# Kernel tuning notes

Hardware: AMD Instinct MI355X
Metric: run time of the kernel (lower is better)

The kernel has to match this reference:

```python
import jax, jax.numpy as jnp
import numpy as np

C = 128        # attention channels (inner_channel)
OUT_C = 256    # bottleneck output channels (in_channel)
NEG = -10000000.0


def conv_bn_relu(x, W, scale, shift):
    """1x1 conv (no bias) + eval-mode BatchNorm folded to scale/shift + ReLU.
    x: [B, Cin, H, W], W: [Cout, Cin]."""
    y = jnp.einsum('oc,bchw->bohw', W, x)
    y = y * scale[None, :, None, None] + shift[None, :, None, None]
    return jax.nn.relu(y)


def setup_inputs() -> dict:
    key = jax.random.key(0)
    ks = jax.random.split(key, 20)
    B, H, W_, K = 4, 128, 128, 1024
    inp = {
        'query_feats': jax.random.normal(ks[0], (B, C, H, W_), jnp.float32),
        'key_feats':   jax.random.normal(ks[1], (B, C, K, 1), jnp.float32),
        'value_feats': jax.random.normal(ks[2], (B, C, K, 1), jnp.float32),
        'key_mask':    jax.random.randint(ks[3], (B, 1, K, 1), 0, 2).astype(bool),
    }
    s = 1.0 / np.sqrt(C)

    def mk(i, cin, cout):
        return (jax.random.normal(ks[i], (cout, cin), jnp.float32) * s,
                jnp.ones((cout,), jnp.float32),
                jnp.zeros((cout,), jnp.float32))

    inp['Wq1'], inp['sq1'], inp['bq1'] = mk(4, C, C)
    inp['Wq2'], inp['sq2'], inp['bq2'] = mk(5, C, C)
    inp['Wk1'], inp['sk1'], inp['bk1'] = mk(6, C, C)
    inp['Wk2'], inp['sk2'], inp['bk2'] = mk(7, C, C)
    inp['Wv'],  inp['sv'],  inp['bv']  = mk(8, C, C)
    inp['Wo'],  inp['so'],  inp['bo']  = mk(9, C, C)
    inp['Wb'],  inp['sb'],  inp['bb']  = mk(10, 2 * C, OUT_C)
    return inp


def reference(query_feats, key_feats, value_feats, key_mask,
              Wq1, sq1, bq1, Wq2, sq2, bq2,
              Wk1, sk1, bk1, Wk2, sk2, bk2,
              Wv, sv, bv, Wo, so, bo, Wb, sb, bb):
    B, _, H, W_ = query_feats.shape
    # projections (2 conv-bn-relu for q/k, 1 for v)
    q = conv_bn_relu(conv_bn_relu(query_feats, Wq1, sq1, bq1), Wq2, sq2, bq2)
    k = conv_bn_relu(conv_bn_relu(key_feats, Wk1, sk1, bk1), Wk2, sk2, bk2)
    v = conv_bn_relu(value_feats, Wv, sv, bv)

    q = q.reshape(B, C, -1).transpose(0, 2, 1)   # [B, HW, C]
    k = k.reshape(B, C, -1)                      # [B, C, K]
    v = v.reshape(B, C, -1).transpose(0, 2, 1)   # [B, K, C]

    sim = jnp.einsum('bqc,bck->bqk', q, k) * (C ** -0.5)   # [B, HW, K]
    m = key_mask.reshape(B, 1, -1).astype(sim.dtype)        # [B, 1, K]
    sim = sim * m + NEG * (1.0 - m)
    attn = jax.nn.softmax(sim, axis=-1)

    ctx = jnp.einsum('bqk,bkc->bqc', attn, v)               # [B, HW, C]
    ctx = ctx.transpose(0, 2, 1).reshape(B, C, H, W_)
    ctx = conv_bn_relu(ctx, Wo, so, bo)                     # out_project

    out = conv_bn_relu(jnp.concatenate([ctx, query_feats], axis=1), Wb, sb, bb)
    return out
```

## Files before the change

### kernel.cpp

```cpp
#include <hip/hip_runtime.h>
#include <hip/hip_bf16.h>

#define B_    4
#define C_    128
#define HW_   16384
#define K_    1024
#define SC2_  0.12751734f
#define NEGL_ (-1.4427e7f)
#define DTHR_ 8.0f

using bf16 = __hip_bfloat16;
typedef __bf16 b8v __attribute__((ext_vector_type(8)));
typedef __bf16 b4v __attribute__((ext_vector_type(4)));
typedef __bf16 b2v __attribute__((ext_vector_type(2)));
typedef float  f4v __attribute__((ext_vector_type(4)));

__device__ __forceinline__ b8v ldb8(const void* p) { return *(const b8v*)p; }
__device__ __forceinline__ b4v ldb4(const void* p) { return *(const b4v*)p; }

#define XSTRIDE 272
#define KSTRIDE 272
#define VSTRIDE 136

__device__ __forceinline__ b8v ldw8(const float* wp, float sc) {
    const float4 a = *(const float4*)wp;
    const float4 c = *(const float4*)(wp + 4);
    b8v r;
    r[0] = (__bf16)(a.x * sc); r[1] = (__bf16)(a.y * sc);
    r[2] = (__bf16)(a.z * sc); r[3] = (__bf16)(a.w * sc);
    r[4] = (__bf16)(c.x * sc); r[5] = (__bf16)(c.y * sc);
    r[6] = (__bf16)(c.z * sc); r[7] = (__bf16)(c.w * sc);
    return r;
}

__global__ __launch_bounds__(256, 2) void prep_kernel(
    const float* __restrict__ query, const float* __restrict__ key, const float* __restrict__ val,
    const float* __restrict__ Wq1, const float* __restrict__ sq1,
    const float* __restrict__ Wq2, const float* __restrict__ sq2,
    const float* __restrict__ Wo,  const float* __restrict__ so,
    const float* __restrict__ Wb,  const float* __restrict__ sb,
    const float* __restrict__ Wk1, const float* __restrict__ sk1, const float* __restrict__ bk1,
    const float* __restrict__ Wk2, const float* __restrict__ sk2, const float* __restrict__ bk2,
    const float* __restrict__ Wv,  const float* __restrict__ sv_, const float* __restrict__ bv,
    bf16* __restrict__ qt, bf16* __restrict__ kbuf, bf16* __restrict__ vbuf,
    __bf16* __restrict__ Wq1p, __bf16* __restrict__ Wq2p,
    __bf16* __restrict__ Wop,  __bf16* __restrict__ Wbp)
{
    __shared__ __align__(16) char SM[69632];
    const int blk = blockIdx.x, t = threadIdx.x;

    if (blk < 32) {
        const int b = blk >> 3, n0 = (blk & 7) * 128;
        const int w = t >> 6, lane = t & 63;
        const int pl = lane & 15, quad = lane >> 4;
        const int ob = 32 * w;
        const int plT = t & 63, cg = t >> 6;
        char*    Xs  = SM;
        __bf16*  Ys  = (__bf16*)(SM + 34816);
        float*   Tmp = (float*)(SM + 34816);

        auto transpose_in = [&](const float* src) {
#pragma unroll
            for (int h = 0; h < 2; ++h) {
                const int p0 = n0 + h * 64;
#pragma unroll 4
                for (int i2 = 0; i2 < 32; ++i2) {
                    const int c = cg * 32 + i2;
                    Tmp[plT * 129 + c] = src[(size_t)(b * 128 + c) * K_ + p0 + plT];
                }
                __syncthreads();
#pragma unroll 4
                for (int it = 0; it < 16; ++it) {
                    const int p = it * 4 + cg;
                    b2v pk2;
                    pk2[0] = (__bf16)Tmp[p * 129 + 2 * plT];
                    pk2[1] = (__bf16)Tmp[p * 129 + 2 * plT + 1];
                    *(b2v*)(Xs + (h * 64 + p) * XSTRIDE + 4 * plT) = pk2;
                }
                __syncthreads();
            }
        };

        transpose_in(key);
        b8v W1f[2][4], W2f[2][4];
#pragma unroll
        for (int mt = 0; mt < 2; ++mt)
#pragma unroll
            for (int s = 0; s < 4; ++s) {
                const int row = ob + mt * 16 + pl;
                W1f[mt][s] = ldw8(Wk1 + row * 128 + s * 32 + quad * 8, sk1[row]);
                W2f[mt][s] = ldw8(Wk2 + row * 128 + s * 32 + quad * 8, sk2[row]);
            }
        {
            f4v acc[2][8];
#pragma unroll
            for (int mt = 0; mt < 2; ++mt)
#pragma unroll
                for (int nt = 0; nt < 8; ++nt) acc[mt][nt] = (f4v){0.f, 0.f, 0.f, 0.f};
#pragma unroll
            for (int s = 0; s < 4; ++s) {
                b8v Bf[8];
#pragma unroll
                for (int nt = 0; nt < 8; ++nt)
                    Bf[nt] = ldb8(Xs + (nt * 16 + pl) * XSTRIDE + s * 64 + quad * 16);
#pragma unroll
                for (int mt = 0; mt < 2; ++mt)
#pragma unroll
                    for (int nt = 0; nt < 8; ++nt)
                        acc[mt][nt] = __builtin_amdgcn_mfma_f32_16x16x32_bf16(W1f[mt][s], Bf[nt], acc[mt][nt], 0, 0, 0);
            }
#pragma unroll
            for (int mt = 0; mt < 2; ++mt) {
                const float4 s4 = *(const float4*)(bk1 + ob + mt * 16 + quad * 4);
                const float shf[4] = {s4.x, s4.y, s4.z, s4.w};
#pragma unroll
                for (int nt = 0; nt < 8; ++nt) {
                    b4v y;
#pragma unroll
                    for (int r = 0; r < 4; ++r) y[r] = (__bf16)fmaxf(acc[mt][nt][r] + shf[r], 0.f);
                    *(b4v*)&Ys[(nt * 16 + pl) * 136 + ob + mt * 16 + quad * 4] = y;
                }
            }
        }
        __syncthreads();
        {
            f4v acc2[2][8];
#pragma unroll
            for (int mt = 0; mt < 2; ++mt)
#pragma unroll
                for (int nt = 0; nt < 8; ++nt) acc2[mt][nt] = (f4v){0.f, 0.f, 0.f, 0.f};
#pragma unroll
            for (int s = 0; s < 4; ++s) {
                b8v Bf[8];
#pragma unroll
                for (int nt = 0; nt < 8; ++nt)
                    Bf[nt] = *(const b8v*)&Ys[(nt * 16 + pl) * 136 + s * 32 + quad * 8];
#pragma unroll
                for (int mt = 0; mt < 2; ++mt)
#pragma unroll
                    for (int nt = 0; nt < 8; ++nt)
                        acc2[mt][nt] = __builtin_amdgcn_mfma_f32_16x16x32_bf16(W2f[mt][s], Bf[nt], acc2[mt][nt], 0, 0, 0);
            }
            bf16* kdst = kbuf + ((size_t)b * K_ + n0) * 128;
#pragma unroll
            for (int mt = 0; mt < 2; ++mt) {
                const float4 s4 = *(const float4*)(bk2 + ob + mt * 16 + quad * 4);
                const float shf[4] = {s4.x, s4.y, s4.z, s4.w};
#pragma unroll
                for (int nt = 0; nt < 8; ++nt) {
                    b4v y;
#pragma unroll
                    for (int r = 0; r < 4; ++r) y[r] = (__bf16)fmaxf(acc2[mt][nt][r] + shf[r], 0.f);
                    *(b4v*)(kdst + (size_t)(nt * 16 + pl) * 128 + ob + mt * 16 + quad * 4) = y;
                }
            }
        }
        __syncthreads();

        transpose_in(val);
        b8v Wvf[2][4];
#pragma unroll
        for (int mt = 0; mt < 2; ++mt)
#pragma unroll
            for (int s = 0; s < 4; ++s) {
                const int row = ob + mt * 16 + pl;
                Wvf[mt][s] = ldw8(Wv + row * 128 + s * 32 + quad * 8, sv_[row]);
            }
        {
            f4v acc[2][8];
#pragma unroll
            for (int mt = 0; mt < 2; ++mt)
#pragma unroll
                for (int nt = 0; nt < 8; ++nt) acc[mt][nt] = (f4v){0.f, 0.f, 0.f, 0.f};
#pragma unroll
            for (int s = 0; s < 4; ++s) {
                b8v Bf[8];
#pragma unroll
                for (int nt = 0; nt < 8; ++nt)
                    Bf[nt] = ldb8(Xs + (nt * 16 + pl) * XSTRIDE + s * 64 + quad * 16);
#pragma unroll
                for (int mt = 0; mt < 2; ++mt)
#pragma unroll
                    for (int nt = 0; nt < 8; ++nt)
                        acc[mt][nt] = __builtin_amdgcn_mfma_f32_16x16x32_bf16(Wvf[mt][s], Bf[nt], acc[mt][nt], 0, 0, 0);
            }
            bf16* vdst = vbuf + (size_t)b * 128 * K_;
#pragma unroll
            for (int mt = 0; mt < 2; ++mt) {
                const float4 s4 = *(const float4*)(bv + ob + mt * 16 + quad * 4);
                const float shf[4] = {s4.x, s4.y, s4.z, s4.w};
#pragma unroll
                for (int nt = 0; nt < 8; ++nt)
#pragma unroll
                    for (int r = 0; r < 4; ++r)
                        vdst[(size_t)(ob + mt * 16 + quad * 4 + r) * K_ + n0 + nt * 16 + pl]
                            = __float2bfloat16(fmaxf(acc[mt][nt][r] + shf[r], 0.f));
            }
        }
    } else if (blk < 1056) {
        float* Xs2 = (float*)SM;
        const int i = blk - 32;
        const int b = i >> 8, p0 = (i & 255) * 64;
        const int pl = t & 63, cg = t >> 6;
#pragma unroll 4
        for (int i2 = 0; i2 < 32; ++i2) {
            const int c = cg * 32 + i2;
            Xs2[pl * 129 + c] = query[(size_t)(b * 128 + c) * HW_ + p0 + pl];
        }
        __syncthreads();
#pragma unroll 4
        for (int it = 0; it < 16; ++it) {
            const int p = it * 4 + cg;
            b2v pk2;
            pk2[0] = (__bf16)Xs2[p * 129 + 2 * pl];
            pk2[1] = (__bf16)Xs2[p * 129 + 2 * pl + 1];
            *(b2v*)(qt + ((size_t)b * HW_ + p0 + p) * 128 + 2 * pl) = pk2;
        }
    } else {
        const int idx = (blk - 1056) * 256 + t;
        if (idx < 16384)      { Wq1p[idx] = (__bf16)(Wq1[idx] * sq1[idx >> 7]); }
        else if (idx < 32768) { const int i2 = idx - 16384; Wq2p[i2] = (__bf16)(Wq2[i2] * sq2[i2 >> 7]); }
        else if (idx < 49152) { const int i2 = idx - 32768; Wop[i2]  = (__bf16)(Wo[i2]  * so[i2 >> 7]); }
        else                  { const int i2 = idx - 49152; Wbp[i2]  = (__bf16)(Wb[i2]  * sb[i2 >> 8]); }
    }
}

__global__ __launch_bounds__(256, 2) void mega_kernel(
    const bf16* __restrict__ qt, const bf16* __restrict__ kbuf, const bf16* __restrict__ vbuf,
    const int* __restrict__ mask,
    const __bf16* __restrict__ Wq1p, const float* __restrict__ bq1,
    const __bf16* __restrict__ Wq2p, const float* __restrict__ bq2,
    const __bf16* __restrict__ Wop,  const float* __restrict__ bo,
    const __bf16* __restrict__ Wbp,  const float* __restrict__ bb,
    float* __restrict__ out)
{
    __shared__ __align__(16) char S[69632];

    const int t = threadIdx.x, w = t >> 6, lane = t & 63;
    const int pl = lane & 15, quad = lane >> 4;
    const int n0 = blockIdx.x * 128;
    const int b  = blockIdx.y;
    const int ob = 32 * w;

    char*   RA  = S;
    __bf16* RAh = (__bf16*)S;
    __bf16* RBh = (__bf16*)(S + 34816);
    char* xl = RA + (t >> 4) * XSTRIDE + (t & 15) * 16;

    {
        const char* qg = (const char*)(qt + ((size_t)b * HW_ + n0) * 128) + t * 16;
#pragma unroll
        for (int i = 0; i < 8; ++i)
            *(float4*)(xl + i * 16 * XSTRIDE) = *(const float4*)(qg + i * 4096);
    }
    {
        b8v W1f[2][4], W2f[2][4];
#pragma unroll
        for (int mt = 0; mt < 2; ++mt)
#pragma unroll
            for (int s = 0; s < 4; ++s) {
                W1f[mt][s] = ldb8(Wq1p + (ob + mt * 16 + pl) * 128 + s * 32 + quad * 8);
                W2f[mt][s] = ldb8(Wq2p + (ob + mt * 16 + pl) * 128 + s * 32 + quad * 8);
            }
        __syncthreads();

        f4v a1[2][8];
#pragma unroll
        for (int mt = 0; mt < 2; ++mt)
#pragma unroll
            for (int nt = 0; nt < 8; ++nt) a1[mt][nt] = (f4v){0.f, 0.f, 0.f, 0.f};
#pragma unroll
        for (int s = 0; s < 4; ++s) {
            b8v Bf[8];
#pragma unroll
            for (int nt = 0; nt < 8; ++nt)
                Bf[nt] = ldb8(RA + (nt * 16 + pl) * XSTRIDE + s * 64 + quad * 16);
#pragma unroll
            for (int mt = 0; mt < 2; ++mt)
#pragma unroll
                for (int nt = 0; nt < 8; ++nt)
                    a1[mt][nt] = __builtin_amdgcn_mfma_f32_16x16x32_bf16(W1f[mt][s], Bf[nt], a1[mt][nt], 0, 0, 0);
        }
#pragma unroll
        for (int mt = 0; mt < 2; ++mt) {
            const float4 s4 = *(const float4*)(bq1 + ob + mt * 16 + quad * 4);
            const float shf[4] = {s4.x, s4.y, s4.z, s4.w};
#pragma unroll
            for (int nt = 0; nt < 8; ++nt) {
                b4v y;
#pragma unroll
                for (int r = 0; r < 4; ++r) y[r] = (__bf16)fmaxf(a1[mt][nt][r] + shf[r], 0.f);
                *(b4v*)&RBh[(nt * 16 + pl) * 136 + ob + mt * 16 + quad * 4] = y;
            }
        }
        __syncthreads();

        f4v a2[2][8];
#pragma unroll
        for (int mt = 0; mt < 2; ++mt)
#pragma unroll
            for (int nt = 0; nt < 8; ++nt) a2[mt][nt] = (f4v){0.f, 0.f, 0.f, 0.f};
#pragma unroll
        for (int s = 0; s < 4; ++s) {
            b8v Bf[8];
#pragma unroll
            for (int nt = 0; nt < 8; ++nt)
                Bf[nt] = *(const b8v*)&RBh[(nt * 16 + pl) * 136 + s * 32 + quad * 8];
#pragma unroll
            for (int mt = 0; mt < 2; ++mt)
#pragma unroll
                for (int nt = 0; nt < 8; ++nt)
                    a2[mt][nt] = __builtin_amdgcn_mfma_f32_16x16x32_bf16(W2f[mt][s], Bf[nt], a2[mt][nt], 0, 0, 0);
        }
#pragma unroll
        for (int mt = 0; mt < 2; ++mt) {
            const float4 s4 = *(const float4*)(bq2 + ob + mt * 16 + quad * 4);
            const float shf[4] = {s4.x, s4.y, s4.z, s4.w};
#pragma unroll
            for (int nt = 0; nt < 8; ++nt) {
                b4v y;
#pragma unroll
                for (int r = 0; r < 4; ++r) y[r] = (__bf16)fmaxf(a2[mt][nt][r] + shf[r], 0.f);
                *(b4v*)&RAh[(nt * 16 + pl) * 136 + ob + mt * 16 + quad * 4] = y;
            }
        }
        __syncthreads();
    }

    b8v qf0[4], qf1[4];
#pragma unroll
    for (int s = 0; s < 4; ++s) {
        qf0[s] = ldb8(RA + (w * 32 + pl) * XSTRIDE + s * 64 + quad * 16);
        qf1[s] = ldb8(RA + (w * 32 + 16 + pl) * XSTRIDE + s * 64 + quad * 16);
    }
    __syncthreads();

    float* bias = (float*)S;
    char* ktile = S + 4096;
    char* vtile = S + 34816;

    for (int i2 = t; i2 < K_; i2 += 256)
        bias[i2] = (mask[b * K_ + i2] != 0) ? 0.f : NEGL_;

    const bf16* kpt = kbuf + (size_t)b * K_ * 128;
    const bf16* vpt = vbuf + (size_t)b * 128 * K_;
    const char* kg = (const char*)kpt + t * 16;
    const char* vg = (const char*)(vpt + (size_t)(t >> 3) * K_) + (t & 7) * 16;
    char* kl = ktile + (t >> 4) * KSTRIDE + (t & 15) * 16;
    char* vl = vtile + (t >> 3) * VSTRIDE + (t & 7) * 16;

    float4 k_r0 = *(const float4*)(kg);
    float4 k_r1 = *(const float4*)(kg + 4096);
    float4 k_r2 = *(const float4*)(kg + 8192);
    float4 k_r3 = *(const float4*)(kg + 12288);
    float4 v_r0 = *(const float4*)(vg);
    float4 v_r1 = *(const float4*)(vg + 65536);
    float4 v_r2 = *(const float4*)(vg + 131072);
    float4 v_r3 = *(const float4*)(vg + 196608);

    f4v ac0[8], ac1[8];
#pragma unroll
    for (int i = 0; i < 8; ++i) { ac0[i] = (f4v){0.f,0.f,0.f,0.f}; ac1[i] = (f4v){0.f,0.f,0.f,0.f}; }
    float mrun0 = -3.0e38f, mrun1 = -3.0e38f, lrun0 = 0.f, lrun1 = 0.f;

#define RAW_BARRIER()                                                 \
    __builtin_amdgcn_sched_barrier(0);                                \
    asm volatile("s_waitcnt lgkmcnt(0)" ::: "memory");                \
    __builtin_amdgcn_s_barrier();                                     \
    __builtin_amdgcn_sched_barrier(0);

    for (int chunk = 0; chunk < 16; ++chunk) {
        const int k0 = chunk * 64;

        *(float4*)(kl)                = k_r0;
        *(float4*)(kl + 16 * KSTRIDE) = k_r1;
        *(float4*)(kl + 32 * KSTRIDE) = k_r2;
        *(float4*)(kl + 48 * KSTRIDE) = k_r3;
        *(float4*)(vl)                = v_r0;
        *(float4*)(vl + 32 * VSTRIDE) = v_r1;
        *(float4*)(vl + 64 * VSTRIDE) = v_r2;
        *(float4*)(vl + 96 * VSTRIDE) = v_r3;
        RAW_BARRIER()

        if (chunk < 15) {
            const char* kgn = kg + (chunk + 1) * 16384;
            const char* vgn = vg + (chunk + 1) * 128;
            k_r0 = *(const float4*)(kgn);
            k_r1 = *(const float4*)(kgn + 4096);
            k_r2 = *(const float4*)(kgn + 8192);
            k_r3 = *(const float4*)(kgn + 12288);
            v_r0 = *(const float4*)(vgn);
            v_r1 = *(const float4*)(vgn + 65536);
            v_r2 = *(const float4*)(vgn + 131072);
            v_r3 = *(const float4*)(vgn + 196608);
        }

        f4v sv0[4], sv1[4];
        __builtin_amdgcn_s_setprio(1);
#pragma unroll
        for (int kt = 0; kt < 4; ++kt) {
            f4v a0 = (f4v){0.f,0.f,0.f,0.f}, a1 = (f4v){0.f,0.f,0.f,0.f};
            const char* krow = ktile + (kt * 16 + pl) * KSTRIDE + quad * 16;
#pragma unroll
            for (int s = 0; s < 4; ++s) {
                const b8v kf = ldb8(krow + s * 64);
                a0 = __builtin_amdgcn_mfma_f32_16x16x32_bf16(kf, qf0[s], a0, 0, 0, 0);
                a1 = __builtin_amdgcn_mfma_f32_16x16x32_bf16(kf, qf1[s], a1, 0, 0, 0);
            }
            const float4 b4 = *(const float4*)&bias[k0 + kt * 16 + quad * 4];
            const float bb4[4] = {b4.x, b4.y, b4.z, b4.w};
#pragma unroll
            for (int r = 0; r < 4; ++r) { sv0[kt][r] = a0[r] * SC2_ + bb4[r];
                                          sv1[kt][r] = a1[r] * SC2_ + bb4[r]; }
        }
        __builtin_amdgcn_s_setprio(0);

        float ml0 = sv0[0][0], ml1 = sv1[0][0];
#pragma unroll
        for (int kt = 0; kt < 4; ++kt)
#pragma unroll
            for (int r = 0; r < 4; ++r) { ml0 = fmaxf(ml0, sv0[kt][r]); ml1 = fmaxf(ml1, sv1[kt][r]); }
        ml0 = fmaxf(ml0, __shfl_xor(ml0, 16, 64)); ml0 = fmaxf(ml0, __shfl_xor(ml0, 32, 64));
        ml1 = fmaxf(ml1, __shfl_xor(ml1, 16, 64)); ml1 = fmaxf(ml1, __shfl_xor(ml1, 32, 64));

        if (__any((ml0 > mrun0 + DTHR_) || (ml1 > mrun1 + DTHR_))) {
            const float mn0 = fmaxf(mrun0, ml0), mn1 = fmaxf(mrun1, ml1);
            const float al0 = exp2f(mrun0 - mn0), al1 = exp2f(mrun1 - mn1);
            lrun0 *= al0; lrun1 *= al1;
            mrun0 = mn0;  mrun1 = mn1;
            float ar0[4], ar1[4];
#pragma unroll
            for (int r = 0; r < 4; ++r) { ar0[r] = __shfl(al0, quad * 4 + r, 64);
                                          ar1[r] = __shfl(al1, quad * 4 + r, 64); }
#pragma unroll
            for (int ct = 0; ct < 8; ++ct)
#pragma unroll
                for (int r = 0; r < 4; ++r) { ac0[ct][r] *= ar0[r]; ac1[ct][r] *= ar1[r]; }
        }

        b4v pk0[4], pk1[4];
        float rs0 = 0.f, rs1 = 0.f;
#pragma unroll
        for (int kt = 0; kt < 4; ++kt)
#pragma unroll
            for (int r = 0; r < 4; ++r) {
                const float p0 = exp2f(sv0[kt][r] - mrun0); rs0 += p0; pk0[kt][r] = (__bf16)p0;
                const float p1 = exp2f(sv1[kt][r] - mrun1); rs1 += p1; pk1[kt][r] = (__bf16)p1;
            }
        rs0 += __shfl_xor(rs0, 16, 64); rs0 += __shfl_xor(rs0, 32, 64);
        rs1 += __shfl_xor(rs1, 16, 64); rs1 += __shfl_xor(rs1, 32, 64);
        lrun0 += rs0; lrun1 += rs1;

        const b8v A00 = __builtin_shufflevector(pk0[0], pk0[1], 0, 1, 2, 3, 4, 5, 6, 7);
        const b8v A01 = __builtin_shufflevector(pk0[2], pk0[3], 0, 1, 2, 3, 4, 5, 6, 7);
        const b8v A10 = __builtin_shufflevector(pk1[0], pk1[1], 0, 1, 2, 3, 4, 5, 6, 7);
        const b8v A11 = __builtin_shufflevector(pk1[2], pk1[3], 0, 1, 2, 3, 4, 5, 6, 7);
        __builtin_amdgcn_s_setprio(1);
#pragma unroll
        for (int ct = 0; ct < 8; ++ct) {
            const char* vrow = vtile + (ct * 16 + pl) * VSTRIDE + quad * 8;
            const b8v B0 = __builtin_shufflevector(ldb4(vrow),      ldb4(vrow + 32), 0, 1, 2, 3, 4, 5, 6, 7);
            const b8v B1 = __builtin_shufflevector(ldb4(vrow + 64), ldb4(vrow + 96), 0, 1, 2, 3, 4, 5, 6, 7);
            ac0[ct] = __builtin_amdgcn_mfma_f32_16x16x32_bf16(A00, B0, ac0[ct], 0, 0, 0);
            ac0[ct] = __builtin_amdgcn_mfma_f32_16x16x32_bf16(A01, B1, ac0[ct], 0, 0, 0);
            ac1[ct] = __builtin_amdgcn_mfma_f32_16x16x32_bf16(A10, B0, ac1[ct], 0, 0, 0);
            ac1[ct] = __builtin_amdgcn_mfma_f32_16x16x32_bf16(A11, B1, ac1[ct], 0, 0, 0);
        }
        __builtin_amdgcn_s_setprio(0);

        RAW_BARRIER()
    }
#undef RAW_BARRIER

    {
        float inv0[4], inv1[4];
#pragma unroll
        for (int r = 0; r < 4; ++r) { inv0[r] = 1.f / __shfl(lrun0, quad * 4 + r, 64);
                                      inv1[r] = 1.f / __shfl(lrun1, quad * 4 + r, 64); }
#pragma unroll
        for (int ct = 0; ct < 8; ++ct)
#pragma unroll
            for (int r = 0; r < 4; ++r) {
                RAh[(w * 32 + quad * 4 + r) * 136 + ct * 16 + pl]      = (__bf16)(ac0[ct][r] * inv0[r]);
                RAh[(w * 32 + 16 + quad * 4 + r) * 136 + ct * 16 + pl] = (__bf16)(ac1[ct][r] * inv1[r]);
            }
    }
    __syncthreads();

    b8v Wof[2][4];
#pragma unroll
    for (int mt = 0; mt < 2; ++mt)
#pragma unroll
        for (int s = 0; s < 4; ++s)
            Wof[mt][s] = ldb8(Wop + (ob + mt * 16 + pl) * 128 + s * 32 + quad * 8);

    const char* qg2 = (const char*)(qt + ((size_t)b * HW_ + n0) * 128) + t * 16;
    float4 q_s0 = *(const float4*)(qg2);
    float4 q_s1 = *(const float4*)(qg2 + 4096);
    float4 q_s2 = *(const float4*)(qg2 + 8192);
    float4 q_s3 = *(const float4*)(qg2 + 12288);
    float4 q_s4 = *(const float4*)(qg2 + 16384);
    float4 q_s5 = *(const float4*)(qg2 + 20480);
    float4 q_s6 = *(const float4*)(qg2 + 24576);
    float4 q_s7 = *(const float4*)(qg2 + 28672);

    {
        f4v f1[2][8];
#pragma unroll
        for (int mt = 0; mt < 2; ++mt)
#pragma unroll
            for (int nt = 0; nt < 8; ++nt) f1[mt][nt] = (f4v){0.f, 0.f, 0.f, 0.f};
#pragma unroll
        for (int s = 0; s < 4; ++s) {
            b8v Bf[8];
#pragma unroll
            for (int nt = 0; nt < 8; ++nt)
                Bf[nt] = ldb8(RA + (nt * 16 + pl) * XSTRIDE + s * 64 + quad * 16);
#pragma unroll
            for (int mt = 0; mt < 2; ++mt)
#pragma unroll
                for (int nt = 0; nt < 8; ++nt)
                    f1[mt][nt] = __builtin_amdgcn_mfma_f32_16x16x32_bf16(Wof[mt][s], Bf[nt], f1[mt][nt], 0, 0, 0);
        }
#pragma unroll
        for (int mt = 0; mt < 2; ++mt) {
            const float4 s4 = *(const float4*)(bo + ob + mt * 16 + quad * 4);
            const float shf[4] = {s4.x, s4.y, s4.z, s4.w};
#pragma unroll
            for (int nt = 0; nt < 8; ++nt) {
                b4v y;
#pragma unroll
                for (int r = 0; r < 4; ++r) y[r] = (__bf16)fmaxf(f1[mt][nt][r] + shf[r], 0.f);
                *(b4v*)&RBh[(nt * 16 + pl) * 136 + ob + mt * 16 + quad * 4] = y;
            }
        }
    }
    __syncthreads();

    *(float4*)(xl)                 = q_s0;
    *(float4*)(xl + 16 * XSTRIDE)  = q_s1;
    *(float4*)(xl + 32 * XSTRIDE)  = q_s2;
    *(float4*)(xl + 48 * XSTRIDE)  = q_s3;
    *(float4*)(xl + 64 * XSTRIDE)  = q_s4;
    *(float4*)(xl + 80 * XSTRIDE)  = q_s5;
    *(float4*)(xl + 96 * XSTRIDE)  = q_s6;
    *(float4*)(xl + 112 * XSTRIDE) = q_s7;
    __syncthreads();

    {
        f4v f2[4][8];
#pragma unroll
        for (int mt = 0; mt < 4; ++mt)
#pragma unroll
            for (int nt = 0; nt < 8; ++nt) f2[mt][nt] = (f4v){0.f, 0.f, 0.f, 0.f};
#pragma unroll
        for (int ks = 0; ks < 8; ++ks) {
            b8v Af[4];
#pragma unroll
            for (int mt = 0; mt < 4; ++mt)
                Af[mt] = ldb8(Wbp + (size_t)(64 * w + mt * 16 + pl) * 256 + ks * 32 + quad * 8);
            b8v Bf[8];
            if (ks < 4) {
#pragma unroll
                for (int nt = 0; nt < 8; ++nt)
                    Bf[nt] = *(const b8v*)&RBh[(nt * 16 + pl) * 136 + ks * 32 + quad * 8];
            } else {
#pragma unroll
                for (int nt = 0; nt < 8; ++nt)
                    Bf[nt] = ldb8(RA + (nt * 16 + pl) * XSTRIDE + (ks - 4) * 64 + quad * 16);
            }
#pragma unroll
            for (int mt = 0; mt < 4; ++mt)
#pragma unroll
                for (int nt = 0; nt < 8; ++nt)
                    f2[mt][nt] = __builtin_amdgcn_mfma_f32_16x16x32_bf16(Af[mt], Bf[nt], f2[mt][nt], 0, 0, 0);
        }
#pragma unroll
        for (int mt = 0; mt < 4; ++mt) {
            const float4 s4 = *(const float4*)(bb + 64 * w + mt * 16 + quad * 4);
            const float shf[4] = {s4.x, s4.y, s4.z, s4.w};
#pragma unroll
            for (int nt = 0; nt < 8; ++nt)
#pragma unroll
                for (int r = 0; r < 4; ++r)
                    out[(size_t)(b * 256 + 64 * w + mt * 16 + quad * 4 + r) * HW_ + n0 + nt * 16 + pl]
                        = fmaxf(f2[mt][nt][r] + shf[r], 0.f);
        }
    }
}

extern "C" void kernel_launch(void* const* d_in, const int* in_sizes, int n_in,
                              void* d_out, int out_size, void* d_ws, size_t ws_size,
                              hipStream_t stream)
{
    const float* query = (const float*)d_in[0];
    const float* key   = (const float*)d_in[1];
    const float* val   = (const float*)d_in[2];
    const int*   mask  = (const int*)  d_in[3];
    const float* Wq1 = (const float*)d_in[4];  const float* sq1 = (const float*)d_in[5];  const float* bq1 = (const float*)d_in[6];
    const float* Wq2 = (const float*)d_in[7];  const float* sq2 = (const float*)d_in[8];  const float* bq2 = (const float*)d_in[9];
    const float* Wk1 = (const float*)d_in[10]; const float* sk1 = (const float*)d_in[11]; const float* bk1 = (const float*)d_in[12];
    const float* Wk2 = (const float*)d_in[13]; const float* sk2 = (const float*)d_in[14]; const float* bk2 = (const float*)d_in[15];
    const float* Wv  = (const float*)d_in[16]; const float* sv  = (const float*)d_in[17]; const float* bv  = (const float*)d_in[18];
    const float* Wo  = (const float*)d_in[19]; const float* so  = (const float*)d_in[20]; const float* bo  = (const float*)d_in[21];
    const float* Wb  = (const float*)d_in[22]; const float* sb  = (const float*)d_in[23]; const float* bb  = (const float*)d_in[24];

    char* ws = (char*)d_ws;
    bf16*   qt   = (bf16*)(ws);
    bf16*   kbuf = (bf16*)(ws + (16u << 20));
    bf16*   vbuf = (bf16*)(ws + (17u << 20));
    char*   wbase = ws + (18u << 20);
    __bf16* Wq1p = (__bf16*)(wbase);
    __bf16* Wq2p = (__bf16*)(wbase + (32u << 10));
    __bf16* Wop  = (__bf16*)(wbase + (64u << 10));
    __bf16* Wbp  = (__bf16*)(wbase + (96u << 10));
    float* outp = (float*)d_out;

    prep_kernel<<<1504, 256, 0, stream>>>(
        query, key, val,
        Wq1, sq1, Wq2, sq2, Wo, so, Wb, sb,
        Wk1, sk1, bk1, Wk2, sk2, bk2, Wv, sv, bv,
        qt, kbuf, vbuf, Wq1p, Wq2p, Wop, Wbp);
    mega_kernel<<<dim3(HW_ / 128, B_), 256, 0, stream>>>(
        qt, kbuf, vbuf, mask,
        Wq1p, bq1, Wq2p, bq2, Wop, bo, Wbp, bb, outp);
}
```

Baseline: 231.3 us.

## Double threads per block so each wave handles 16 query rows

The fused attention kernel now launches 512 threads (8 waves) per block instead of 256. Each wave owns 16 query rows and 16 output channels instead of 32, and the global-to-LDS copies are split across the larger thread count. The aim is more resident waves per CU to hide latency, since LDS use limits a CU to two blocks. In exchange, each K/V element read from LDS feeds half as many MFMAs, so LDS traffic per FLOP rises. The tight launch bound (512, 4) may also cap registers low enough to cause spills.

```diff
diff --git a/kernel.cpp b/kernel.cpp
--- a/kernel.cpp
+++ b/kernel.cpp
@@ -225,7 +225,7 @@
     }
 }
 
-__global__ __launch_bounds__(256, 2) void mega_kernel(
+__global__ __launch_bounds__(512, 4) void mega_kernel(
     const bf16* __restrict__ qt, const bf16* __restrict__ kbuf, const bf16* __restrict__ vbuf,
     const int* __restrict__ mask,
     const __bf16* __restrict__ Wq1p, const float* __restrict__ bq1,
@@ -240,7 +240,7 @@
     const int pl = lane & 15, quad = lane >> 4;
     const int n0 = blockIdx.x * 128;
     const int b  = blockIdx.y;
-    const int ob = 32 * w;
+    const int ob = 16 * w;
 
     char*   RA  = S;
     __bf16* RAh = (__bf16*)S;
@@ -250,25 +250,21 @@
     {
         const char* qg = (const char*)(qt + ((size_t)b * HW_ + n0) * 128) + t * 16;
 #pragma unroll
-        for (int i = 0; i < 8; ++i)
-            *(float4*)(xl + i * 16 * XSTRIDE) = *(const float4*)(qg + i * 4096);
+        for (int i = 0; i < 4; ++i)
+            *(float4*)(xl + i * 32 * XSTRIDE) = *(const float4*)(qg + i * 8192);
     }
     {
-        b8v W1f[2][4], W2f[2][4];
-#pragma unroll
-        for (int mt = 0; mt < 2; ++mt)
-#pragma unroll
-            for (int s = 0; s < 4; ++s) {
-                W1f[mt][s] = ldb8(Wq1p + (ob + mt * 16 + pl) * 128 + s * 32 + quad * 8);
-                W2f[mt][s] = ldb8(Wq2p + (ob + mt * 16 + pl) * 128 + s * 32 + quad * 8);
-            }
+        b8v W1f[4], W2f[4];
+#pragma unroll
+        for (int s = 0; s < 4; ++s) {
+            W1f[s] = ldb8(Wq1p + (ob + pl) * 128 + s * 32 + quad * 8);
+            W2f[s] = ldb8(Wq2p + (ob + pl) * 128 + s * 32 + quad * 8);
+        }
         __syncthreads();
 
-        f4v a1[2][8];
-#pragma unroll
-        for (int mt = 0; mt < 2; ++mt)
-#pragma unroll
-            for (int nt = 0; nt < 8; ++nt) a1[mt][nt] = (f4v){0.f, 0.f, 0.f, 0.f};
+        f4v a1[8];
+#pragma unroll
+        for (int nt = 0; nt < 8; ++nt) a1[nt] = (f4v){0.f, 0.f, 0.f, 0.f};
 #pragma unroll
         for (int s = 0; s < 4; ++s) {
             b8v Bf[8];
@@ -276,30 +272,25 @@
             for (int nt = 0; nt < 8; ++nt)
                 Bf[nt] = ldb8(RA + (nt * 16 + pl) * XSTRIDE + s * 64 + quad * 16);
 #pragma unroll
-            for (int mt = 0; mt < 2; ++mt)
-#pragma unroll
-                for (int nt = 0; nt < 8; ++nt)
-                    a1[mt][nt] = __builtin_amdgcn_mfma_f32_16x16x32_bf16(W1f[mt][s], Bf[nt], a1[mt][nt], 0, 0, 0);
-        }
-#pragma unroll
-        for (int mt = 0; mt < 2; ++mt) {
-            const float4 s4 = *(const float4*)(bq1 + ob + mt * 16 + quad * 4);
+            for (int nt = 0; nt < 8; ++nt)
+                a1[nt] = __builtin_amdgcn_mfma_f32_16x16x32_bf16(W1f[s], Bf[nt], a1[nt], 0, 0, 0);
+        }
+        {
+            const float4 s4 = *(const float4*)(bq1 + ob + quad * 4);
             const float shf[4] = {s4.x, s4.y, s4.z, s4.w};
 #pragma unroll
             for (int nt = 0; nt < 8; ++nt) {
                 b4v y;
 #pragma unroll
-                for (int r = 0; r < 4; ++r) y[r] = (__bf16)fmaxf(a1[mt][nt][r] + shf[r], 0.f);
-                *(b4v*)&RBh[(nt * 16 + pl) * 136 + ob + mt * 16 + quad * 4] = y;
+                for (int r = 0; r < 4; ++r) y[r] = (__bf16)fmaxf(a1[nt][r] + shf[r], 0.f);
+                *(b4v*)&RBh[(nt * 16 + pl) * 136 + ob + quad * 4] = y;
             }
         }
         __syncthreads();
 
-        f4v a2[2][8];
-#pragma unroll
-        for (int mt = 0; mt < 2; ++mt)
-#pragma unroll
-            for (int nt = 0; nt < 8; ++nt) a2[mt][nt] = (f4v){0.f, 0.f, 0.f, 0.f};
+        f4v a2[8];
+#pragma unroll
+        for (int nt = 0; nt < 8; ++nt) a2[nt] = (f4v){0.f, 0.f, 0.f, 0.f};
 #pragma unroll
         for (int s = 0; s < 4; ++s) {
             b8v Bf[8];
@@ -307,39 +298,34 @@
             for (int nt = 0; nt < 8; ++nt)
                 Bf[nt] = *(const b8v*)&RBh[(nt * 16 + pl) * 136 + s * 32 + quad * 8];
 #pragma unroll
-            for (int mt = 0; mt < 2; ++mt)
-#pragma unroll
-                for (int nt = 0; nt < 8; ++nt)
-                    a2[mt][nt] = __builtin_amdgcn_mfma_f32_16x16x32_bf16(W2f[mt][s], Bf[nt], a2[mt][nt], 0, 0, 0);
-        }
-#pragma unroll
-        for (int mt = 0; mt < 2; ++mt) {
-            const float4 s4 = *(const float4*)(bq2 + ob + mt * 16 + quad * 4);
+            for (int nt = 0; nt < 8; ++nt)
+                a2[nt] = __builtin_amdgcn_mfma_f32_16x16x32_bf16(W2f[s], Bf[nt], a2[nt], 0, 0, 0);
+        }
+        {
+            const float4 s4 = *(const float4*)(bq2 + ob + quad * 4);
             const float shf[4] = {s4.x, s4.y, s4.z, s4.w};
 #pragma unroll
             for (int nt = 0; nt < 8; ++nt) {
                 b4v y;
 #pragma unroll
-                for (int r = 0; r < 4; ++r) y[r] = (__bf16)fmaxf(a2[mt][nt][r] + shf[r], 0.f);
-                *(b4v*)&RAh[(nt * 16 + pl) * 136 + ob + mt * 16 + quad * 4] = y;
+                for (int r = 0; r < 4; ++r) y[r] = (__bf16)fmaxf(a2[nt][r] + shf[r], 0.f);
+                *(b4v*)&RAh[(nt * 16 + pl) * 136 + ob + quad * 4] = y;
             }
         }
         __syncthreads();
     }
 
-    b8v qf0[4], qf1[4];
-#pragma unroll
-    for (int s = 0; s < 4; ++s) {
-        qf0[s] = ldb8(RA + (w * 32 + pl) * XSTRIDE + s * 64 + quad * 16);
-        qf1[s] = ldb8(RA + (w * 32 + 16 + pl) * XSTRIDE + s * 64 + quad * 16);
-    }
+    b8v qf[4];
+#pragma unroll
+    for (int s = 0; s < 4; ++s)
+        qf[s] = ldb8(RA + (w * 16 + pl) * XSTRIDE + s * 64 + quad * 16);
     __syncthreads();
 
     float* bias = (float*)S;
     char* ktile = S + 4096;
     char* vtile = S + 34816;
 
-    for (int i2 = t; i2 < K_; i2 += 256)
+    for (int i2 = t; i2 < K_; i2 += 512)
         bias[i2] = (mask[b * K_ + i2] != 0) ? 0.f : NEGL_;
 
     const bf16* kpt = kbuf + (size_t)b * K_ * 128;
@@ -350,18 +336,14 @@
     char* vl = vtile + (t >> 3) * VSTRIDE + (t & 7) * 16;
 
     float4 k_r0 = *(const float4*)(kg);
-    float4 k_r1 = *(const float4*)(kg + 4096);
-    float4 k_r2 = *(const float4*)(kg + 8192);
-    float4 k_r3 = *(const float4*)(kg + 12288);
+    float4 k_r1 = *(const float4*)(kg + 8192);
     float4 v_r0 = *(const float4*)(vg);
-    float4 v_r1 = *(const float4*)(vg + 65536);
-    float4 v_r2 = *(const float4*)(vg + 131072);
-    float4 v_r3 = *(const float4*)(vg + 196608);
-
-    f4v ac0[8], ac1[8];
-#pragma unroll
-    for (int i = 0; i < 8; ++i) { ac0[i] = (f4v){0.f,0.f,0.f,0.f}; ac1[i] = (f4v){0.f,0.f,0.f,0.f}; }
-    float mrun0 = -3.0e38f, mrun1 = -3.0e38f, lrun0 = 0.f, lrun1 = 0.f;
+    float4 v_r1 = *(const float4*)(vg + 131072);
+
+    f4v ac[8];
+#pragma unroll
+    for (int i = 0; i < 8; ++i) ac[i] = (f4v){0.f, 0.f, 0.f, 0.f};
+    float mrun = -3.0e38f, lrun = 0.f;
 
 #define RAW_BARRIER()                                                 \
     __builtin_amdgcn_sched_barrier(0);                                \
@@ -373,98 +355,78 @@
         const int k0 = chunk * 64;
 
         *(float4*)(kl)                = k_r0;
-        *(float4*)(kl + 16 * KSTRIDE) = k_r1;
-        *(float4*)(kl + 32 * KSTRIDE) = k_r2;
-        *(float4*)(kl + 48 * KSTRIDE) = k_r3;
+        *(float4*)(kl + 32 * KSTRIDE) = k_r1;
         *(float4*)(vl)                = v_r0;
-        *(float4*)(vl + 32 * VSTRIDE) = v_r1;
-        *(float4*)(vl + 64 * VSTRIDE) = v_r2;
-        *(float4*)(vl + 96 * VSTRIDE) = v_r3;
+        *(float4*)(vl + 64 * VSTRIDE) = v_r1;
         RAW_BARRIER()
 
         if (chunk < 15) {
             const char* kgn = kg + (chunk + 1) * 16384;
             const char* vgn = vg + (chunk + 1) * 128;
             k_r0 = *(const float4*)(kgn);
-            k_r1 = *(const float4*)(kgn + 4096);
-            k_r2 = *(const float4*)(kgn + 8192);
-            k_r3 = *(const float4*)(kgn + 12288);
+            k_r1 = *(const float4*)(kgn + 8192);
             v_r0 = *(const float4*)(vgn);
-            v_r1 = *(const float4*)(vgn + 65536);
-            v_r2 = *(const float4*)(vgn + 131072);
-            v_r3 = *(const float4*)(vgn + 196608);
-        }
-
-        f4v sv0[4], sv1[4];
+            v_r1 = *(const float4*)(vgn + 131072);
+        }
+
+        f4v sv[4];
         __builtin_amdgcn_s_setprio(1);
 #pragma unroll
         for (int kt = 0; kt < 4; ++kt) {
-            f4v a0 = (f4v){0.f,0.f,0.f,0.f}, a1 = (f4v){0.f,0.f,0.f,0.f};
+            f4v a = (f4v){0.f, 0.f, 0.f, 0.f};
             const char* krow = ktile + (kt * 16 + pl) * KSTRIDE + quad * 16;
 #pragma unroll
-            for (int s = 0; s < 4; ++s) {
-                const b8v kf = ldb8(krow + s * 64);
-                a0 = __builtin_amdgcn_mfma_f32_16x16x32_bf16(kf, qf0[s], a0, 0, 0, 0);
-                a1 = __builtin_amdgcn_mfma_f32_16x16x32_bf16(kf, qf1[s], a1, 0, 0, 0);
-            }
+            for (int s = 0; s < 4; ++s)
+                a = __builtin_amdgcn_mfma_f32_16x16x32_bf16(ldb8(krow + s * 64), qf[s], a, 0, 0, 0);
             const float4 b4 = *(const float4*)&bias[k0 + kt * 16 + quad * 4];
             const float bb4[4] = {b4.x, b4.y, b4.z, b4.w};
 #pragma unroll
-            for (int r = 0; r < 4; ++r) { sv0[kt][r] = a0[r] * SC2_ + bb4[r];
-                                          sv1[kt][r] = a1[r] * SC2_ + bb4[r]; }
+            for (int r = 0; r < 4; ++r) sv[kt][r] = a[r] * SC2_ + bb4[r];
         }
         __builtin_amdgcn_s_setprio(0);
 
-        float ml0 = sv0[0][0], ml1 = sv1[0][0];
+        float ml = sv[0][0];
 #pragma unroll
         for (int kt = 0; kt < 4; ++kt)
 #pragma unroll
-            for (int r = 0; r < 4; ++r) { ml0 = fmaxf(ml0, sv0[kt][r]); ml1 = fmaxf(ml1, sv1[kt][r]); }
-        ml0 = fmaxf(ml0, __shfl_xor(ml0, 16, 64)); ml0 = fmaxf(ml0, __shfl_xor(ml0, 32, 64));
-        ml1 = fmaxf(ml1, __shfl_xor(ml1, 16, 64)); ml1 = fmaxf(ml1, __shfl_xor(ml1, 32, 64));
-
-        if (__any((ml0 > mrun0 + DTHR_) || (ml1 > mrun1 + DTHR_))) {
-            const float mn0 = fmaxf(mrun0, ml0), mn1 = fmaxf(mrun1, ml1);
-            const float al0 = exp2f(mrun0 - mn0), al1 = exp2f(mrun1 - mn1);
-            lrun0 *= al0; lrun1 *= al1;
-            mrun0 = mn0;  mrun1 = mn1;
-            float ar0[4], ar1[4];
-#pragma unroll
-            for (int r = 0; r < 4; ++r) { ar0[r] = __shfl(al0, quad * 4 + r, 64);
-                                          ar1[r] = __shfl(al1, quad * 4 + r, 64); }
+            for (int r = 0; r < 4; ++r) ml = fmaxf(ml, sv[kt][r]);
+        ml = fmaxf(ml, __shfl_xor(ml, 16, 64));
+        ml = fmaxf(ml, __shfl_xor(ml, 32, 64));
+
+        if (__any(ml > mrun + DTHR_)) {
+            const float mn = fmaxf(mrun, ml);
+            const float al = exp2f(mrun - mn);
+            lrun *= al; mrun = mn;
+            float ar[4];
+#pragma unroll
+            for (int r = 0; r < 4; ++r) ar[r] = __shfl(al, quad * 4 + r, 64);
 #pragma unroll
             for (int ct = 0; ct < 8; ++ct)
 #pragma unroll
-                for (int r = 0; r < 4; ++r) { ac0[ct][r] *= ar0[r]; ac1[ct][r] *= ar1[r]; }
-        }
-
-        b4v pk0[4], pk1[4];
-        float rs0 = 0.f, rs1 = 0.f;
+                for (int r = 0; r < 4; ++r) ac[ct][r] *= ar[r];
+        }
+
+        b4v pk[4];
+        float rs = 0.f;
 #pragma unroll
         for (int kt = 0; kt < 4; ++kt)
 #pragma unroll
             for (int r = 0; r < 4; ++r) {
-                const float p0 = exp2f(sv0[kt][r] - mrun0); rs0 += p0; pk0[kt][r] = (__bf16)p0;
-                const float p1 = exp2f(sv1[kt][r] - mrun1); rs1 += p1; pk1[kt][r] = (__bf16)p1;
-            }
-        rs0 += __shfl_xor(rs0, 16, 64); rs0 += __shfl_xor(rs0, 32, 64);
-        rs1 += __shfl_xor(rs1, 16, 64); rs1 += __shfl_xor(rs1, 32, 64);
-        lrun0 += rs0; lrun1 += rs1;
-
-        const b8v A00 = __builtin_shufflevector(pk0[0], pk0[1], 0, 1, 2, 3, 4, 5, 6, 7);
-        const b8v A01 = __builtin_shufflevector(pk0[2], pk0[3], 0, 1, 2, 3, 4, 5, 6, 7);
-        const b8v A10 = __builtin_shufflevector(pk1[0], pk1[1], 0, 1, 2, 3, 4, 5, 6, 7);
-        const b8v A11 = __builtin_shufflevector(pk1[2], pk1[3], 0, 1, 2, 3, 4, 5, 6, 7);
+                const float p = exp2f(sv[kt][r] - mrun); rs += p; pk[kt][r] = (__bf16)p;
+            }
+        rs += __shfl_xor(rs, 16, 64); rs += __shfl_xor(rs, 32, 64);
+        lrun += rs;
+
+        const b8v A0 = __builtin_shufflevector(pk[0], pk[1], 0, 1, 2, 3, 4, 5, 6, 7);
+        const b8v A1 = __builtin_shufflevector(pk[2], pk[3], 0, 1, 2, 3, 4, 5, 6, 7);
         __builtin_amdgcn_s_setprio(1);
 #pragma unroll
         for (int ct = 0; ct < 8; ++ct) {
             const char* vrow = vtile + (ct * 16 + pl) * VSTRIDE + quad * 8;
             const b8v B0 = __builtin_shufflevector(ldb4(vrow),      ldb4(vrow + 32), 0, 1, 2, 3, 4, 5, 6, 7);
             const b8v B1 = __builtin_shufflevector(ldb4(vrow + 64), ldb4(vrow + 96), 0, 1, 2, 3, 4, 5, 6, 7);
-            ac0[ct] = __builtin_amdgcn_mfma_f32_16x16x32_bf16(A00, B0, ac0[ct], 0, 0, 0);
-            ac0[ct] = __builtin_amdgcn_mfma_f32_16x16x32_bf16(A01, B1, ac0[ct], 0, 0, 0);
-            ac1[ct] = __builtin_amdgcn_mfma_f32_16x16x32_bf16(A10, B0, ac1[ct], 0, 0, 0);
-            ac1[ct] = __builtin_amdgcn_mfma_f32_16x16x32_bf16(A11, B1, ac1[ct], 0, 0, 0);
+            ac[ct] = __builtin_amdgcn_mfma_f32_16x16x32_bf16(A0, B0, ac[ct], 0, 0, 0);
+            ac[ct] = __builtin_amdgcn_mfma_f32_16x16x32_bf16(A1, B1, ac[ct], 0, 0, 0);
         }
         __builtin_amdgcn_s_setprio(0);
 
@@ -473,43 +435,32 @@
 #undef RAW_BARRIER
 
     {
-        float inv0[4], inv1[4];
-#pragma unroll
-        for (int r = 0; r < 4; ++r) { inv0[r] = 1.f / __shfl(lrun0, quad * 4 + r, 64);
-                                      inv1[r] = 1.f / __shfl(lrun1, quad * 4 + r, 64); }
+        float inv[4];
+#pragma unroll
+        for (int r = 0; r < 4; ++r) inv[r] = 1.f / __shfl(lrun, quad * 4 + r, 64);
 #pragma unroll
         for (int ct = 0; ct < 8; ++ct)
 #pragma unroll
-            for (int r = 0; r < 4; ++r) {
-                RAh[(w * 32 + quad * 4 + r) * 136 + ct * 16 + pl]      = (__bf16)(ac0[ct][r] * inv0[r]);
-                RAh[(w * 32 + 16 + quad * 4 + r) * 136 + ct * 16 + pl] = (__bf16)(ac1[ct][r] * inv1[r]);
-            }
+            for (int r = 0; r < 4; ++r)
+                RAh[(w * 16 + quad * 4 + r) * 136 + ct * 16 + pl] = (__bf16)(ac[ct][r] * inv[r]);
     }
     __syncthreads();
 
-    b8v Wof[2][4];
-#pragma unroll
-    for (int mt = 0; mt < 2; ++mt)
-#pragma unroll
-        for (int s = 0; s < 4; ++s)
-            Wof[mt][s] = ldb8(Wop + (ob + mt * 16 + pl) * 128 + s * 32 + quad * 8);
+    b8v Wof[4];
+#pragma unroll
+    for (int s = 0; s < 4; ++s)
+        Wof[s] = ldb8(Wop + (ob + pl) * 128 + s * 32 + quad * 8);
 
     const char* qg2 = (const char*)(qt + ((size_t)b * HW_ + n0) * 128) + t * 16;
     float4 q_s0 = *(const float4*)(qg2);
-    float4 q_s1 = *(const float4*)(qg2 + 4096);
-    float4 q_s2 = *(const float4*)(qg2 + 8192);
-    float4 q_s3 = *(const float4*)(qg2 + 12288);
-    float4 q_s4 = *(const float4*)(qg2 + 16384);
-    float4 q_s5 = *(const float4*)(qg2 + 20480);
-    float4 q_s6 = *(const float4*)(qg2 + 24576);
-    float4 q_s7 = *(const float4*)(qg2 + 28672);
+    float4 q_s1 = *(const float4*)(qg2 + 8192);
+    float4 q_s2 = *(const float4*)(qg2 + 16384);
+    float4 q_s3 = *(const float4*)(qg2 + 24576);
 
     {
-        f4v f1[2][8];
-#pragma unroll
-        for (int mt = 0; mt < 2; ++mt)
-#pragma unroll
-            for (int nt = 0; nt < 8; ++nt) f1[mt][nt] = (f4v){0.f, 0.f, 0.f, 0.f};
+        f4v f1[8];
+#pragma unroll
+        for (int nt = 0; nt < 8; ++nt) f1[nt] = (f4v){0.f, 0.f, 0.f, 0.f};
 #pragma unroll
         for (int s = 0; s < 4; ++s) {
             b8v Bf[8];
@@ -517,48 +468,41 @@
             for (int nt = 0; nt < 8; ++nt)
                 Bf[nt] = ldb8(RA + (nt * 16 + pl) * XSTRIDE + s * 64 + quad * 16);
 #pragma unroll
-            for (int mt = 0; mt < 2; ++mt)
-#pragma unroll
-                for (int nt = 0; nt < 8; ++nt)
-                    f1[mt][nt] = __builtin_amdgcn_mfma_f32_16x16x32_bf16(Wof[mt][s], Bf[nt], f1[mt][nt], 0, 0, 0);
-        }
-#pragma unroll
-        for (int mt = 0; mt < 2; ++mt) {
-            const float4 s4 = *(const float4*)(bo + ob + mt * 16 + quad * 4);
+            for (int nt = 0; nt < 8; ++nt)
+                f1[nt] = __builtin_amdgcn_mfma_f32_16x16x32_bf16(Wof[s], Bf[nt], f1[nt], 0, 0, 0);
+        }
+        {
+            const float4 s4 = *(const float4*)(bo + ob + quad * 4);
             const float shf[4] = {s4.x, s4.y, s4.z, s4.w};
 #pragma unroll
             for (int nt = 0; nt < 8; ++nt) {
                 b4v y;
 #pragma unroll
-                for (int r = 0; r < 4; ++r) y[r] = (__bf16)fmaxf(f1[mt][nt][r] + shf[r], 0.f);
-                *(b4v*)&RBh[(nt * 16 + pl) * 136 + ob + mt * 16 + quad * 4] = y;
+                for (int r = 0; r < 4; ++r) y[r] = (__bf16)fmaxf(f1[nt][r] + shf[r], 0.f);
+                *(b4v*)&RBh[(nt * 16 + pl) * 136 + ob + quad * 4] = y;
             }
         }
     }
     __syncthreads();
 
     *(float4*)(xl)                 = q_s0;
-    *(float4*)(xl + 16 * XSTRIDE)  = q_s1;
-    *(float4*)(xl + 32 * XSTRIDE)  = q_s2;
-    *(float4*)(xl + 48 * XSTRIDE)  = q_s3;
-    *(float4*)(xl + 64 * XSTRIDE)  = q_s4;
-    *(float4*)(xl + 80 * XSTRIDE)  = q_s5;
-    *(float4*)(xl + 96 * XSTRIDE)  = q_s6;
-    *(float4*)(xl + 112 * XSTRIDE) = q_s7;
+    *(float4*)(xl + 32 * XSTRIDE)  = q_s1;
+    *(float4*)(xl + 64 * XSTRIDE)  = q_s2;
+    *(float4*)(xl + 96 * XSTRIDE)  = q_s3;
     __syncthreads();
 
     {
-        f4v f2[4][8];
-#pragma unroll
-        for (int mt = 0; mt < 4; ++mt)
+        f4v f2[2][8];
+#pragma unroll
+        for (int mt = 0; mt < 2; ++mt)
 #pragma unroll
             for (int nt = 0; nt < 8; ++nt) f2[mt][nt] = (f4v){0.f, 0.f, 0.f, 0.f};
 #pragma unroll
         for (int ks = 0; ks < 8; ++ks) {
-            b8v Af[4];
-#pragma unroll
-            for (int mt = 0; mt < 4; ++mt)
-                Af[mt] = ldb8(Wbp + (size_t)(64 * w + mt * 16 + pl) * 256 + ks * 32 + quad * 8);
+            b8v Af[2];
+#pragma unroll
+            for (int mt = 0; mt < 2; ++mt)
+                Af[mt] = ldb8(Wbp + (size_t)(32 * w + mt * 16 + pl) * 256 + ks * 32 + quad * 8);
             b8v Bf[8];
             if (ks < 4) {
 #pragma unroll
@@ -570,20 +514,20 @@
                     Bf[nt] = ldb8(RA + (nt * 16 + pl) * XSTRIDE + (ks - 4) * 64 + quad * 16);
             }
 #pragma unroll
-            for (int mt = 0; mt < 4; ++mt)
+            for (int mt = 0; mt < 2; ++mt)
 #pragma unroll
                 for (int nt = 0; nt < 8; ++nt)
                     f2[mt][nt] = __builtin_amdgcn_mfma_f32_16x16x32_bf16(Af[mt], Bf[nt], f2[mt][nt], 0, 0, 0);
         }
 #pragma unroll
-        for (int mt = 0; mt < 4; ++mt) {
-            const float4 s4 = *(const float4*)(bb + 64 * w + mt * 16 + quad * 4);
+        for (int mt = 0; mt < 2; ++mt) {
+            const float4 s4 = *(const float4*)(bb + 32 * w + mt * 16 + quad * 4);
             const float shf[4] = {s4.x, s4.y, s4.z, s4.w};
 #pragma unroll
             for (int nt = 0; nt < 8; ++nt)
 #pragma unroll
                 for (int r = 0; r < 4; ++r)
-                    out[(size_t)(b * 256 + 64 * w + mt * 16 + quad * 4 + r) * HW_ + n0 + nt * 16 + pl]
+                    out[(size_t)(b * 256 + 32 * w + mt * 16 + quad * 4 + r) * HW_ + n0 + nt * 16 + pl]
                         = fmaxf(f2[mt][nt][r] + shf[r], 0.f);
         }
     }
@@ -621,7 +565,7 @@
         Wq1, sq1, Wq2, sq2, Wo, so, Wb, sb,
         Wk1, sk1, bk1, Wk2, sk2, bk2, Wv, sv, bv,
         qt, kbuf, vbuf, Wq1p, Wq2p, Wop, Wbp);
-    mega_kernel<<<dim3(HW_ / 128, B_), 256, 0, stream>>>(
+    mega_kernel<<<dim3(HW_ / 128, B_), 512, 0, stream>>>(
         qt, kbuf, vbuf, mask,
         Wq1p, bq1, Wq2p, bq2, Wop, bo, Wbp, bb, outp);
 }
```

New measurement: 221.3 us. 1.04x faster.
